# Optimization experiments

Measured on AMD Instinct MI355X. Metric: run time of the kernel, lower is better.

The kernel has to match this reference:

```python
import jax, jax.numpy as jnp
import numpy as np

HID = 128
N_NODES = 50000
N_EDGES = 640000
N_GRAPHS = 64
N_LAYERS = 3
LN_EPS = 1e-5


def _ln(h, g, b):
    mu = jnp.mean(h, axis=-1, keepdims=True)
    v = jnp.mean(jnp.square(h - mu), axis=-1, keepdims=True)
    return (h - mu) * jax.lax.rsqrt(v + LN_EPS) * g + b


def _mlp2(h, W1, b1, g, be, W2, b2):
    # Linear -> ReLU -> LayerNorm -> (Dropout=identity in eval) -> Linear
    h = _ln(jax.nn.relu(h @ W1.T + b1), g, be)
    return h @ W2.T + b2


def _forward(x, edge_index, batch, axis_W1, axis_b1, axis_g, axis_be, axis_W2, axis_b2, org_W1, org_b1, org_g, org_be, org_W2, org_b2, nin_W, nin_b, conv_W1, conv_b1, conv_g, conv_be, conv_W2, conv_b2, eps, ln_g, ln_b, gate_W1, gate_b1, gate_g, gate_be, gate_W2, gate_b2, head_W1, head_b1, head_g, head_be, head_W2, head_b2):
    axis = x[:, 9:12]
    origin = x[:, 12:15]
    others = jnp.concatenate([x[:, :9], x[:, 15:19]], axis=1)  # [N, 13]
    axis_z = _mlp2(axis, axis_W1, axis_b1, axis_g, axis_be, axis_W2, axis_b2)
    org_z = _mlp2(origin, org_W1, org_b1, org_g, org_be, org_W2, org_b2)
    h = jnp.concatenate([others, axis_z, org_z], axis=1) @ nin_W.T + nin_b  # [N, HID]
    src, dst = edge_index[0], edge_index[1]
    n = x.shape[0]
    for l in range(N_LAYERS):
        res = h
        # GIN: sum-aggregate source features into targets (gather + scatter-add)
        agg = jax.ops.segment_sum(h[src], dst, num_segments=n)
        m = (1.0 + eps[l]) * h + agg
        m = _mlp2(m, conv_W1[l], conv_b1[l], conv_g[l], conv_be[l], conv_W2[l], conv_b2[l])
        h = _ln(jax.nn.relu(m), ln_g[l], ln_b[l]) + res
    # AttentionalAggregation: segment softmax over per-graph node gates
    gate = _mlp2(h, gate_W1, gate_b1, gate_g, gate_be, gate_W2, gate_b2)  # [N, 1]
    gmax = jax.ops.segment_max(gate, batch, num_segments=N_GRAPHS)
    e = jnp.exp(gate - gmax[batch])
    denom = jax.ops.segment_sum(e, batch, num_segments=N_GRAPHS)
    attn = e / denom[batch]
    g = jax.ops.segment_sum(attn * h, batch, num_segments=N_GRAPHS)  # [B, HID]
    logit = _mlp2(g, head_W1, head_b1, head_g, head_be, head_W2, head_b2)[:, 0]
    return logit


def setup_inputs() -> dict:
    key = jax.random.key(0)
    ks = iter(jax.random.split(key, 64))
    nk = lambda: next(ks)
    lin = lambda o, i: jax.random.normal(nk(), (o, i), jnp.float32) / np.float32(np.sqrt(i))
    lin3 = lambda L, o, i: jnp.stack([lin(o, i) for _ in range(L)])
    z = lambda *s: jnp.zeros(s, jnp.float32)
    o = lambda *s: jnp.ones(s, jnp.float32)
    inp = {}
    inp['x'] = jax.random.normal(nk(), (N_NODES, 19), jnp.float32)
    inp['edge_index'] = jax.random.randint(nk(), (2, N_EDGES), 0, N_NODES)
    inp['batch'] = jnp.sort(jax.random.randint(nk(), (N_NODES,), 0, N_GRAPHS))
    for p in ('axis', 'org'):
        inp[p + '_W1'] = lin(16, 3); inp[p + '_b1'] = z(16)
        inp[p + '_g'] = o(16); inp[p + '_be'] = z(16)
        inp[p + '_W2'] = lin(16, 16); inp[p + '_b2'] = z(16)
    inp['nin_W'] = lin(HID, 45); inp['nin_b'] = z(HID)
    inp['conv_W1'] = lin3(N_LAYERS, HID, HID); inp['conv_b1'] = z(N_LAYERS, HID)
    inp['conv_g'] = o(N_LAYERS, HID); inp['conv_be'] = z(N_LAYERS, HID)
    inp['conv_W2'] = lin3(N_LAYERS, HID, HID); inp['conv_b2'] = z(N_LAYERS, HID)
    inp['eps'] = z(N_LAYERS)
    inp['ln_g'] = o(N_LAYERS, HID); inp['ln_b'] = z(N_LAYERS, HID)
    for p in ('gate', 'head'):
        inp[p + '_W1'] = lin(HID // 2, HID); inp[p + '_b1'] = z(HID // 2)
        inp[p + '_g'] = o(HID // 2); inp[p + '_be'] = z(HID // 2)
        inp[p + '_W2'] = lin(1, HID // 2); inp[p + '_b2'] = z(1)
    return inp


def reference(x, edge_index, batch, axis_W1, axis_b1, axis_g, axis_be, axis_W2, axis_b2, org_W1, org_b1, org_g, org_be, org_W2, org_b2, nin_W, nin_b, conv_W1, conv_b1, conv_g, conv_be, conv_W2, conv_b2, eps, ln_g, ln_b, gate_W1, gate_b1, gate_g, gate_be, gate_W2, gate_b2, head_W1, head_b1, head_g, head_be, head_W2, head_b2):
    return _forward(x, edge_index, batch, axis_W1, axis_b1, axis_g, axis_be, axis_W2, axis_b2, org_W1, org_b1, org_g, org_be, org_W2, org_b2, nin_W, nin_b, conv_W1, conv_b1, conv_g, conv_be, conv_W2, conv_b2, eps, ln_g, ln_b, gate_W1, gate_b1, gate_g, gate_be, gate_W2, gate_b2, head_W1, head_b1, head_g, head_be, head_W2, head_b2)
```

## Files before the change

kernel.cpp:

```cpp
#include <hip/hip_runtime.h>

#define N_NODESC 50000
#define N_EDGESC 640000
#define N_GRAPHSC 64
#define HIDC 128
#define LN_EPSF 1e-5f
#define POOL_SPLIT 16
#define NGRID_GB ((N_NODESC + 255) / 256)
#define NGRID64 ((N_NODESC + 63) / 64)
#define PREP_ELEMS (8192 + 49152 + 49152)
#define WPREP_NB ((PREP_ELEMS + 255) / 256)
#define B1C 200
#define BCHUNK 3200
#define NBUK 98
#define WBUK 512

typedef short bf16x8 __attribute__((ext_vector_type(8)));
typedef float f32x4 __attribute__((ext_vector_type(4)));

static __device__ __forceinline__ unsigned ord_enc(float f) {
  unsigned u = __float_as_uint(f);
  return (u & 0x80000000u) ? ~u : (u | 0x80000000u);
}
static __device__ __forceinline__ float ord_dec(unsigned u) {
  return __uint_as_float((u & 0x80000000u) ? (u ^ 0x80000000u) : ~u);
}
static __device__ __forceinline__ unsigned short f2bf(float x) {
  unsigned u = __float_as_uint(x);
  u += 0x7fffu + ((u >> 16) & 1u);
  return (unsigned short)(u >> 16);
}
static __device__ __forceinline__ float bf2f(unsigned short b) {
  return __uint_as_float(((unsigned)b) << 16);
}

static __device__ __forceinline__ void mlp16(float in0, float in1, float in2,
    const float* __restrict__ W1, const float* __restrict__ b1,
    const float* __restrict__ g, const float* __restrict__ be,
    const float* __restrict__ W2, const float* __restrict__ b2,
    float* __restrict__ out) {
  float h[16];
  float s1 = 0.f, s2 = 0.f;
#pragma unroll
  for (int j = 0; j < 16; ++j) {
    float v = b1[j] + W1[j*3+0]*in0 + W1[j*3+1]*in1 + W1[j*3+2]*in2;
    v = fmaxf(v, 0.f);
    h[j] = v; s1 += v; s2 += v*v;
  }
  float mu = s1 * (1.f/16.f);
  float var = fmaxf(s2 * (1.f/16.f) - mu*mu, 0.f);
  float rs = rsqrtf(var + LN_EPSF);
  float z[16];
#pragma unroll
  for (int j = 0; j < 16; ++j) z[j] = (h[j]-mu)*rs*g[j] + be[j];
#pragma unroll
  for (int j = 0; j < 16; ++j) {
    float v = b2[j];
#pragma unroll
    for (int k = 0; k < 16; ++k) v += W2[j*16+k]*z[k];
    out[j] = v;
  }
}

__global__ __launch_bounds__(256) void bin_count_kernel(const int* __restrict__ ei,
    int* __restrict__ counts, const int* __restrict__ batch, int* __restrict__ gstart,
    const float* __restrict__ ninW, unsigned short* __restrict__ ninWb,
    const float* __restrict__ cW1, unsigned short* __restrict__ cW1b,
    const float* __restrict__ cW2, unsigned short* __restrict__ cW2b) {
  const int b = blockIdx.x;
  if (b < B1C) {
    __shared__ int cnt[NBUK];
    for (int i = threadIdx.x; i < NBUK; i += 256) cnt[i] = 0;
    __syncthreads();
    const int e0 = b * BCHUNK;
    const int e1 = e0 + BCHUNK;
    for (int e = e0 + threadIdx.x; e < e1; e += 256)
      atomicAdd(&cnt[ei[N_EDGESC + e] >> 9], 1);
    __syncthreads();
    for (int i = threadIdx.x; i < NBUK; i += 256)
      counts[i * B1C + b] = cnt[i];
  } else if (b < B1C + NGRID_GB) {
    int i = (b - B1C) * 256 + threadIdx.x;
    if (i >= N_NODESC) return;
    int bb_ = batch[i];
    int prev = (i == 0) ? -1 : batch[i-1];
    for (int g = prev + 1; g <= bb_; ++g) gstart[g] = i;
    if (i == N_NODESC - 1) {
      for (int g = bb_ + 1; g <= N_GRAPHSC; ++g) gstart[g] = N_NODESC;
    }
  } else {
    int i = (b - B1C - NGRID_GB) * 256 + threadIdx.x;
    if (i < 8192) {
      int f = i >> 6, k = i & 63;
      ninWb[i] = (k < 45) ? f2bf(ninW[f*45 + k]) : (unsigned short)0;
    } else if (i < 8192 + 49152) {
      int j = i - 8192;
      cW1b[j] = f2bf(cW1[j]);
    } else if (i < PREP_ELEMS) {
      int j = i - 8192 - 49152;
      cW2b[j] = f2bf(cW2[j]);
    }
  }
}

__global__ __launch_bounds__(256) void bin_scanA_kernel(const int* __restrict__ counts,
                                                        int* __restrict__ offl,
                                                        int* __restrict__ btot) {
  const int buk = blockIdx.x, t = threadIdx.x;
  const int lane = t & 63, w = t >> 6;
  int v = (t < B1C) ? counts[buk * B1C + t] : 0;
  const int orig = v;
#pragma unroll
  for (int off = 1; off < 64; off <<= 1) {
    int n = __shfl_up(v, off);
    if (lane >= off) v += n;
  }
  __shared__ int wsum[4];
  if (lane == 63) wsum[w] = v;
  __syncthreads();
  if (t == 0) {
    int run = 0;
#pragma unroll
    for (int k = 0; k < 4; ++k) { int x = wsum[k]; wsum[k] = run; run += x; }
  }
  __syncthreads();
  int incl = v + wsum[w];
  if (t < B1C) offl[buk * B1C + t] = incl - orig;
  if (t == 255) btot[buk] = incl;
}

__global__ __launch_bounds__(128) void bin_scanB_kernel(const int* __restrict__ btot,
                                                        int* __restrict__ bb) {
  const int t = threadIdx.x, lane = t & 63, w = t >> 6;
  int v = (t < NBUK) ? btot[t] : 0;
  const int orig = v;
#pragma unroll
  for (int off = 1; off < 64; off <<= 1) {
    int n = __shfl_up(v, off);
    if (lane >= off) v += n;
  }
  __shared__ int ws2[2];
  if (lane == 63) ws2[w] = v;
  __syncthreads();
  int add = (w == 1) ? ws2[0] : 0;
  int excl = v + add - orig;
  if (t < NBUK) bb[t] = excl;
  if (t == 0) bb[NBUK] = N_EDGESC;
}

__global__ __launch_bounds__(256, 4) void bin_write_enc_kernel(
    const int* __restrict__ ei, const int* __restrict__ offl, const int* __restrict__ bb,
    int2* __restrict__ pairs,
    const float* __restrict__ x,
    const float* __restrict__ aW1, const float* __restrict__ ab1,
    const float* __restrict__ ag,  const float* __restrict__ abe,
    const float* __restrict__ aW2, const float* __restrict__ ab2,
    const float* __restrict__ oW1, const float* __restrict__ ob1,
    const float* __restrict__ og,  const float* __restrict__ obe,
    const float* __restrict__ oW2, const float* __restrict__ ob2,
    const unsigned short* __restrict__ ninWb, const float* __restrict__ ninb,
    unsigned short* __restrict__ Hb) {
  __shared__ unsigned short Ab[64*136];
  const int t = threadIdx.x;

  if (blockIdx.x < B1C) {
    int* cur = (int*)Ab;
    const int blk = blockIdx.x;
    for (int i = t; i < NBUK; i += 256) cur[i] = bb[i] + offl[i * B1C + blk];
    __syncthreads();
    const int e0 = blk * BCHUNK;
    const int e1 = e0 + BCHUNK;
    for (int e = e0 + t; e < e1; e += 256) {
      int s = ei[e], d = ei[N_EDGESC + e];
      int pos = atomicAdd(&cur[d >> 9], 1);
      pairs[pos] = make_int2(s, d);
    }
    return;
  }

  const int nb = (blockIdx.x - B1C) * 64;

  if (t < 192) {
    const int n = t & 63;
    const int gn = nb + n;
    const int grp = t >> 6;
    if (gn < N_NODESC) {
      const float* xr = x + gn * 19;
      if (grp == 0) {
        float z[16];
        mlp16(xr[9], xr[10], xr[11], aW1, ab1, ag, abe, aW2, ab2, z);
#pragma unroll
        for (int k = 0; k < 16; ++k) Ab[n*136 + 13 + k] = f2bf(z[k]);
      } else if (grp == 1) {
        float z[16];
        mlp16(xr[12], xr[13], xr[14], oW1, ob1, og, obe, oW2, ob2, z);
#pragma unroll
        for (int k = 0; k < 16; ++k) Ab[n*136 + 29 + k] = f2bf(z[k]);
      } else {
#pragma unroll
        for (int k = 0; k < 9; ++k) Ab[n*136 + k] = f2bf(xr[k]);
#pragma unroll
        for (int k = 0; k < 4; ++k) Ab[n*136 + 9 + k] = f2bf(xr[15 + k]);
#pragma unroll
        for (int k = 45; k < 64; ++k) Ab[n*136 + k] = 0;
      }
    } else {
      if (grp == 0) {
#pragma unroll
        for (int k = 0; k < 16; ++k) Ab[n*136 + 13 + k] = 0;
      } else if (grp == 1) {
#pragma unroll
        for (int k = 0; k < 16; ++k) Ab[n*136 + 29 + k] = 0;
      } else {
#pragma unroll
        for (int k = 0; k < 13; ++k) Ab[n*136 + k] = 0;
#pragma unroll
        for (int k = 45; k < 64; ++k) Ab[n*136 + k] = 0;
      }
    }
  }
  __syncthreads();

  const int lane = t & 63, wv = t >> 6;
  const int quad = lane >> 4, l16 = lane & 15;
  const int arow = (wv*16 + l16)*136 + quad*8;
  f32x4 acc[8];
#pragma unroll
  for (int ft = 0; ft < 8; ++ft) acc[ft] = (f32x4){0.f,0.f,0.f,0.f};
#pragma unroll
  for (int ks = 0; ks < 2; ++ks) {
    bf16x8 a = *(const bf16x8*)(const void*)&Ab[arow + ks*32];
#pragma unroll
    for (int ft = 0; ft < 8; ++ft) {
      bf16x8 bfr = *(const bf16x8*)&ninWb[(ft*16 + l16)*64 + quad*8 + ks*32];
      acc[ft] = __builtin_amdgcn_mfma_f32_16x16x32_bf16(a, bfr, acc[ft], 0, 0, 0);
    }
  }
  float bbv[8];
#pragma unroll
  for (int ft = 0; ft < 8; ++ft) bbv[ft] = ninb[ft*16 + l16];
  __syncthreads();
#pragma unroll
  for (int r = 0; r < 4; ++r) {
    int nloc = wv*16 + quad*4 + r;
#pragma unroll
    for (int ft = 0; ft < 8; ++ft)
      Ab[nloc*136 + ft*16 + l16] = f2bf(acc[ft][r] + bbv[ft]);
  }
  __syncthreads();
#pragma unroll
  for (int i = 0; i < 4; ++i) {
    int chunk = t + i*256;
    int n = chunk >> 4, c8 = chunk & 15;
    int gn = nb + n;
    if (gn < N_NODESC)
      *(bf16x8*)&Hb[gn*HIDC + c8*8] = *(const bf16x8*)&Ab[n*136 + c8*8];
  }
}

__global__ __launch_bounds__(256) void bucket_build_kernel(const int2* __restrict__ pairs,
    const int* __restrict__ bb, int* __restrict__ rowptr, int* __restrict__ esrc) {
  __shared__ int hist[WBUK];
  __shared__ int wsum[4];
  __shared__ int totS;
  const int b = blockIdx.x, t = threadIdx.x;
  const int lane = t & 63, w = t >> 6;
  const int node0 = b * WBUK;
  for (int i = t; i < WBUK; i += 256) hist[i] = 0;
  __syncthreads();
  const int base = bb[b], end = bb[b + 1];
  for (int p = base + t; p < end; p += 256)
    atomicAdd(&hist[pairs[p].y - node0], 1);
  __syncthreads();
  const int v0 = hist[t], v1 = hist[256 + t];
  int a = v0;
#pragma unroll
  for (int off = 1; off < 64; off <<= 1) {
    int n = __shfl_up(a, off);
    if (lane >= off) a += n;
  }
  if (lane == 63) wsum[w] = a;
  __syncthreads();
  if (t == 0) {
    int run = 0;
#pragma unroll
    for (int k = 0; k < 4; ++k) { int x = wsum[k]; wsum[k] = run; run += x; }
    totS = run;
  }
  __syncthreads();
  const int e0 = a + wsum[w] - v0;
  const int tot0 = totS;
  __syncthreads();
  int c = v1;
#pragma unroll
  for (int off = 1; off < 64; off <<= 1) {
    int n = __shfl_up(c, off);
    if (lane >= off) c += n;
  }
  if (lane == 63) wsum[w] = c;
  __syncthreads();
  if (t == 0) {
    int run = 0;
#pragma unroll
    for (int k = 0; k < 4; ++k) { int x = wsum[k]; wsum[k] = run; run += x; }
  }
  __syncthreads();
  const int e1 = tot0 + c + wsum[w] - v1;
  hist[t] = e0;
  hist[256 + t] = e1;
  const int n0 = node0 + t, n1 = node0 + 256 + t;
  if (n0 < N_NODESC) rowptr[n0] = base + e0;
  if (n1 < N_NODESC) rowptr[n1] = base + e1;
  __syncthreads();
  for (int p = base + t; p < end; p += 256) {
    int2 pr = pairs[p];
    int slot = base + atomicAdd(&hist[pr.y - node0], 1);
    esrc[slot] = pr.x;
  }
  if (b == NBUK - 1 && t == 0) rowptr[N_NODESC] = N_EDGESC;
}

__global__ __launch_bounds__(128) void agg_kernel(const unsigned short* __restrict__ Hb,
    const int* __restrict__ rowptr, const int* __restrict__ esrc,
    const float* __restrict__ epsp, unsigned short* __restrict__ Mb) {
  const int t = threadIdx.x;
  const int c8 = t & 15;
  const int v  = t >> 4;
  const int node = blockIdx.x * 8 + v;
  if (node >= N_NODESC) return;
  const float e1 = 1.0f + epsp[0];
  bf16x8 h = *(const bf16x8*)&Hb[node*HIDC + c8*8];
  float acc[8];
#pragma unroll
  for (int k = 0; k < 8; ++k) acc[k] = 0.f;
  int s = rowptr[node];
  const int e = rowptr[node+1];
  for (; s + 8 <= e; s += 8) {
    int i0 = esrc[s],   i1 = esrc[s+1], i2 = esrc[s+2], i3 = esrc[s+3];
    int i4 = esrc[s+4], i5 = esrc[s+5], i6 = esrc[s+6], i7 = esrc[s+7];
    bf16x8 x0 = *(const bf16x8*)&Hb[i0*HIDC + c8*8];
    bf16x8 x1 = *(const bf16x8*)&Hb[i1*HIDC + c8*8];
    bf16x8 x2 = *(const bf16x8*)&Hb[i2*HIDC + c8*8];
    bf16x8 x3 = *(const bf16x8*)&Hb[i3*HIDC + c8*8];
    bf16x8 x4 = *(const bf16x8*)&Hb[i4*HIDC + c8*8];
    bf16x8 x5 = *(const bf16x8*)&Hb[i5*HIDC + c8*8];
    bf16x8 x6 = *(const bf16x8*)&Hb[i6*HIDC + c8*8];
    bf16x8 x7 = *(const bf16x8*)&Hb[i7*HIDC + c8*8];
#pragma unroll
    for (int k = 0; k < 8; ++k)
      acc[k] += ((bf2f((unsigned short)x0[k]) + bf2f((unsigned short)x1[k]))
               + (bf2f((unsigned short)x2[k]) + bf2f((unsigned short)x3[k])))
              + ((bf2f((unsigned short)x4[k]) + bf2f((unsigned short)x5[k]))
               + (bf2f((unsigned short)x6[k]) + bf2f((unsigned short)x7[k])));
  }
  for (; s + 4 <= e; s += 4) {
    int i0 = esrc[s], i1 = esrc[s+1], i2 = esrc[s+2], i3 = esrc[s+3];
    bf16x8 x0 = *(const bf16x8*)&Hb[i0*HIDC + c8*8];
    bf16x8 x1 = *(const bf16x8*)&Hb[i1*HIDC + c8*8];
    bf16x8 x2 = *(const bf16x8*)&Hb[i2*HIDC + c8*8];
    bf16x8 x3 = *(const bf16x8*)&Hb[i3*HIDC + c8*8];
#pragma unroll
    for (int k = 0; k < 8; ++k)
      acc[k] += (bf2f((unsigned short)x0[k]) + bf2f((unsigned short)x1[k]))
              + (bf2f((unsigned short)x2[k]) + bf2f((unsigned short)x3[k]));
  }
  for (; s < e; ++s) {
    bf16x8 x0 = *(const bf16x8*)&Hb[esrc[s]*HIDC + c8*8];
#pragma unroll
    for (int k = 0; k < 8; ++k) acc[k] += bf2f((unsigned short)x0[k]);
  }
  bf16x8 m8;
#pragma unroll
  for (int k = 0; k < 8; ++k)
    m8[k] = (short)f2bf(e1*bf2f((unsigned short)h[k]) + acc[k]);
  *(bf16x8*)&Mb[node*HIDC + c8*8] = m8;
}

template<bool GATE>
__global__ __launch_bounds__(256, 3) void gemmpair_kernel(
    const unsigned short* __restrict__ Mb,
    const unsigned short* __restrict__ Hin,
    const unsigned short* __restrict__ W1b, const float* __restrict__ b1,
    const float* __restrict__ g1, const float* __restrict__ be1,
    const unsigned short* __restrict__ W2b, const float* __restrict__ b2,
    const float* __restrict__ lng, const float* __restrict__ lnb,
    unsigned short* __restrict__ Hout,
    const float* __restrict__ gW1, const float* __restrict__ gb1,
    const float* __restrict__ glng, const float* __restrict__ glnb,
    const float* __restrict__ gW2, const float* __restrict__ gb2,
    const int* __restrict__ batch, float* __restrict__ gateb,
    unsigned* __restrict__ gmaxu) {
  __shared__ unsigned short Ab[64*136];
  __shared__ unsigned short Wl[128*136];
  __shared__ unsigned sgm[N_GRAPHSC];
  const int t = threadIdx.x;
  const int nb = blockIdx.x * 64;
  if (GATE && t < N_GRAPHSC) sgm[t] = 0u;

#pragma unroll
  for (int i = 0; i < 4; ++i) {
    int chunk = t + i*256;
    int n = chunk >> 4, c8 = chunk & 15;
    int gn = nb + n;
    bf16x8 v = {0,0,0,0,0,0,0,0};
    if (gn < N_NODESC) v = *(const bf16x8*)&Mb[gn*HIDC + c8*8];
    *(bf16x8*)&Ab[n*136 + c8*8] = v;
  }
#pragma unroll
  for (int i = 0; i < 8; ++i) {
    int q = t + i*256;
    int f = q >> 4, c8 = q & 15;
    *(bf16x8*)&Wl[f*136 + c8*8] = *(const bf16x8*)&W1b[f*HIDC + c8*8];
  }
  __syncthreads();

  const int lane = t & 63, wv = t >> 6;
  const int quad = lane >> 4, l16 = lane & 15;
  const int arow = (wv*16 + l16)*136 + quad*8;

  f32x4 acc[8];
#pragma unroll
  for (int ft = 0; ft < 8; ++ft) acc[ft] = (f32x4){0.f,0.f,0.f,0.f};
#pragma unroll
  for (int ks = 0; ks < 4; ++ks) {
    bf16x8 a = *(const bf16x8*)(const void*)&Ab[arow + ks*32];
#pragma unroll
    for (int ft = 0; ft < 8; ++ft) {
      bf16x8 b = *(const bf16x8*)(const void*)&Wl[(ft*16 + l16)*136 + quad*8 + ks*32];
      acc[ft] = __builtin_amdgcn_mfma_f32_16x16x32_bf16(a, b, acc[ft], 0, 0, 0);
    }
  }

  {
    float bbv[8], gg[8], bee[8];
#pragma unroll
    for (int ft = 0; ft < 8; ++ft) {
      int f = ft*16 + l16;
      bbv[ft] = b1[f]; gg[ft] = g1[f]; bee[ft] = be1[f];
    }
    float s1[4] = {0,0,0,0}, s2[4] = {0,0,0,0};
#pragma unroll
    for (int ft = 0; ft < 8; ++ft)
#pragma unroll
      for (int r = 0; r < 4; ++r) {
        float v = fmaxf(acc[ft][r] + bbv[ft], 0.f);
        acc[ft][r] = v; s1[r] += v; s2[r] += v*v;
      }
#pragma unroll
    for (int m = 1; m < 16; m <<= 1)
#pragma unroll
      for (int r = 0; r < 4; ++r) {
        s1[r] += __shfl_xor(s1[r], m);
        s2[r] += __shfl_xor(s2[r], m);
      }
    float mu[4], rs[4];
#pragma unroll
    for (int r = 0; r < 4; ++r) {
      mu[r] = s1[r] * (1.f/128.f);
      float var = fmaxf(s2[r] * (1.f/128.f) - mu[r]*mu[r], 0.f);
      rs[r] = rsqrtf(var + LN_EPSF);
    }
    __syncthreads();
#pragma unroll
    for (int r = 0; r < 4; ++r) {
      int nloc = wv*16 + quad*4 + r;
#pragma unroll
      for (int ft = 0; ft < 8; ++ft) {
        float o = (acc[ft][r] - mu[r])*rs[r]*gg[ft] + bee[ft];
        Ab[nloc*136 + ft*16 + l16] = f2bf(o);
      }
    }
  }
#pragma unroll
  for (int i = 0; i < 8; ++i) {
    int q = t + i*256;
    int f = q >> 4, c8 = q & 15;
    *(bf16x8*)&Wl[f*136 + c8*8] = *(const bf16x8*)&W2b[f*HIDC + c8*8];
  }
  __syncthreads();

#pragma unroll
  for (int ft = 0; ft < 8; ++ft) acc[ft] = (f32x4){0.f,0.f,0.f,0.f};
#pragma unroll
  for (int ks = 0; ks < 4; ++ks) {
    bf16x8 a = *(const bf16x8*)(const void*)&Ab[arow + ks*32];
#pragma unroll
    for (int ft = 0; ft < 8; ++ft) {
      bf16x8 b = *(const bf16x8*)(const void*)&Wl[(ft*16 + l16)*136 + quad*8 + ks*32];
      acc[ft] = __builtin_amdgcn_mfma_f32_16x16x32_bf16(a, b, acc[ft], 0, 0, 0);
    }
  }

  {
    float bbv[8], gg[8], bee[8];
#pragma unroll
    for (int ft = 0; ft < 8; ++ft) {
      int f = ft*16 + l16;
      bbv[ft] = b2[f]; gg[ft] = lng[f]; bee[ft] = lnb[f];
    }
    float s1[4] = {0,0,0,0}, s2[4] = {0,0,0,0};
#pragma unroll
    for (int ft = 0; ft < 8; ++ft)
#pragma unroll
      for (int r = 0; r < 4; ++r) {
        float v = fmaxf(acc[ft][r] + bbv[ft], 0.f);
        acc[ft][r] = v; s1[r] += v; s2[r] += v*v;
      }
#pragma unroll
    for (int m = 1; m < 16; m <<= 1)
#pragma unroll
      for (int r = 0; r < 4; ++r) {
        s1[r] += __shfl_xor(s1[r], m);
        s2[r] += __shfl_xor(s2[r], m);
      }
    float mu[4], rs[4];
#pragma unroll
    for (int r = 0; r < 4; ++r) {
      mu[r] = s1[r] * (1.f/128.f);
      float var = fmaxf(s2[r] * (1.f/128.f) - mu[r]*mu[r], 0.f);
      rs[r] = rsqrtf(var + LN_EPSF);
    }
    __syncthreads();
#pragma unroll
    for (int r = 0; r < 4; ++r) {
      int nloc = wv*16 + quad*4 + r;
#pragma unroll
      for (int ft = 0; ft < 8; ++ft) {
        float o = (acc[ft][r] - mu[r])*rs[r]*gg[ft] + bee[ft];
        Ab[nloc*136 + ft*16 + l16] = f2bf(o);
      }
    }
  }
  __syncthreads();
#pragma unroll
  for (int i = 0; i < 4; ++i) {
    int chunk = t + i*256;
    int n = chunk >> 4, cc = chunk & 15;
    int gn = nb + n;
    bf16x8 o8 = {0,0,0,0,0,0,0,0};
    if (gn < N_NODESC) {
      bf16x8 vv = *(const bf16x8*)&Ab[n*136 + cc*8];
      bf16x8 rr = *(const bf16x8*)&Hin[gn*HIDC + cc*8];
#pragma unroll
      for (int k = 0; k < 8; ++k)
        o8[k] = (short)f2bf(bf2f((unsigned short)vv[k]) + bf2f((unsigned short)rr[k]));
      *(bf16x8*)&Hout[gn*HIDC + cc*8] = o8;
    }
    if (GATE) *(bf16x8*)&Ab[n*136 + cc*8] = o8;
  }

  if (GATE) {
#pragma unroll
    for (int i = 0; i < 8; ++i) {
      int q = t + i*256;
      int f = q >> 5, c4 = q & 31;
      float4 v = *(const float4*)&gW1[f*HIDC + c4*4];
      ushort4 hh;
      hh.x = f2bf(v.x); hh.y = f2bf(v.y); hh.z = f2bf(v.z); hh.w = f2bf(v.w);
      *(ushort4*)&Wl[f*136 + c4*4] = hh;
    }
    __syncthreads();

    f32x4 gacc[4];
#pragma unroll
    for (int ft = 0; ft < 4; ++ft) gacc[ft] = (f32x4){0.f,0.f,0.f,0.f};
#pragma unroll
    for (int ks = 0; ks < 4; ++ks) {
      bf16x8 a = *(const bf16x8*)(const void*)&Ab[arow + ks*32];
#pragma unroll
      for (int ft = 0; ft < 4; ++ft) {
        bf16x8 b = *(const bf16x8*)(const void*)&Wl[(ft*16 + l16)*136 + quad*8 + ks*32];
        gacc[ft] = __builtin_amdgcn_mfma_f32_16x16x32_bf16(a, b, gacc[ft], 0, 0, 0);
      }
    }

    float bbv[4], gg[4], bee[4], w2v[4];
#pragma unroll
    for (int ft = 0; ft < 4; ++ft) {
      int f = ft*16 + l16;
      bbv[ft] = gb1[f]; gg[ft] = glng[f]; bee[ft] = glnb[f]; w2v[ft] = gW2[f];
    }
    float s1[4] = {0,0,0,0}, s2[4] = {0,0,0,0};
#pragma unroll
    for (int ft = 0; ft < 4; ++ft)
#pragma unroll
      for (int r = 0; r < 4; ++r) {
        float v = fmaxf(gacc[ft][r] + bbv[ft], 0.f);
        gacc[ft][r] = v; s1[r] += v; s2[r] += v*v;
      }
#pragma unroll
    for (int m = 1; m < 16; m <<= 1)
#pragma unroll
      for (int r = 0; r < 4; ++r) {
        s1[r] += __shfl_xor(s1[r], m);
        s2[r] += __shfl_xor(s2[r], m);
      }
    float pd[4];
#pragma unroll
    for (int r = 0; r < 4; ++r) {
      float mu = s1[r] * (1.f/64.f);
      float var = fmaxf(s2[r] * (1.f/64.f) - mu*mu, 0.f);
      float rs = rsqrtf(var + LN_EPSF);
      float p = 0.f;
#pragma unroll
      for (int ft = 0; ft < 4; ++ft)
        p += ((gacc[ft][r] - mu)*rs*gg[ft] + bee[ft]) * w2v[ft];
      pd[r] = p;
    }
#pragma unroll
    for (int m = 1; m < 16; m <<= 1)
#pragma unroll
      for (int r = 0; r < 4; ++r) pd[r] += __shfl_xor(pd[r], m);
    if (l16 == 0) {
      float b2v = gb2[0];
#pragma unroll
      for (int r = 0; r < 4; ++r) {
        int node = nb + wv*16 + quad*4 + r;
        if (node < N_NODESC) {
          float gv = pd[r] + b2v;
          gateb[node] = gv;
          atomicMax(&sgm[batch[node]], ord_enc(gv));
        }
      }
    }
    __syncthreads();
    if (t < N_GRAPHSC && sgm[t] != 0u) atomicMax(&gmaxu[t], sgm[t]);
  }
}

__global__ __launch_bounds__(256) void pool_kernel(const unsigned short* __restrict__ Hb,
    const float* __restrict__ gateb, const int* __restrict__ gstart,
    const unsigned* __restrict__ gmaxu, float* __restrict__ S,
    float* __restrict__ denom) {
  const int g    = blockIdx.x / POOL_SPLIT;
  const int part = blockIdx.x % POOL_SPLIT;
  const int s0 = gstart[g], s1 = gstart[g+1];
  const int cnt = s1 - s0;
  const int chunk = (cnt + POOL_SPLIT - 1) / POOL_SPLIT;
  int lo = s0 + part * chunk;
  int hi = lo + chunk; if (hi > s1) hi = s1;
  const int t = threadIdx.x;
  const int c8 = t & 15;
  const int v  = t >> 4;
  const float gm = ord_dec(gmaxu[g]);
  float acc[8];
#pragma unroll
  for (int k = 0; k < 8; ++k) acc[k] = 0.f;
  float de = 0.f;
  for (int n = lo + v; n < hi; n += 16) {
    float e = expf(gateb[n] - gm);
    bf16x8 hv = *(const bf16x8*)&Hb[n*HIDC + c8*8];
#pragma unroll
    for (int k = 0; k < 8; ++k) acc[k] += e * bf2f((unsigned short)hv[k]);
    if (c8 == 0) de += e;
  }
  __shared__ float sacc[16*128];
  __shared__ float sden[16];
#pragma unroll
  for (int k = 0; k < 8; ++k) sacc[v*128 + c8*8 + k] = acc[k];
  if (c8 == 0) sden[v] = de;
  __syncthreads();
  if (t < 128) {
    float s = 0.f;
#pragma unroll
    for (int vv = 0; vv < 16; ++vv) s += sacc[vv*128 + t];
    atomicAdd(&S[g*HIDC + t], s);
  }
  if (t == 0) {
    float d = 0.f;
#pragma unroll
    for (int vv = 0; vv < 16; ++vv) d += sden[vv];
    atomicAdd(&denom[g], d);
  }
}

__global__ __launch_bounds__(64) void head_kernel(const float* __restrict__ S,
    const float* __restrict__ denom, const float* __restrict__ W1,
    const float* __restrict__ b1, const float* __restrict__ g,
    const float* __restrict__ be, const float* __restrict__ W2,
    const float* __restrict__ b2, float* __restrict__ out) {
  const int gr = blockIdx.x;
  const int j = threadIdx.x;
  const float inv = 1.0f / denom[gr];
  float v = b1[j];
  for (int k = 0; k < HIDC; ++k) v += (S[gr*HIDC + k] * inv) * W1[j*HIDC + k];
  v = fmaxf(v, 0.f);
  float s1 = v, s2 = v*v;
  for (int off = 32; off; off >>= 1) { s1 += __shfl_xor(s1, off); s2 += __shfl_xor(s2, off); }
  float mu = s1 * (1.f/64.f);
  float var = fmaxf(s2 * (1.f/64.f) - mu*mu, 0.f);
  float rs = rsqrtf(var + LN_EPSF);
  float z = (v-mu)*rs*g[j] + be[j];
  float p = z * W2[j];
  for (int off = 32; off; off >>= 1) p += __shfl_xor(p, off);
  if (j == 0) out[gr] = p + b2[0];
}

extern "C" void kernel_launch(void* const* d_in, const int* in_sizes, int n_in,
                              void* d_out, int out_size, void* d_ws, size_t ws_size,
                              hipStream_t stream) {
  (void)in_sizes; (void)n_in; (void)out_size; (void)ws_size;
  const float* x     = (const float*)d_in[0];
  const int*   ei    = (const int*)d_in[1];
  const int*   batch = (const int*)d_in[2];
  const float* aW1 = (const float*)d_in[3];
  const float* ab1 = (const float*)d_in[4];
  const float* ag  = (const float*)d_in[5];
  const float* abe = (const float*)d_in[6];
  const float* aW2 = (const float*)d_in[7];
  const float* ab2 = (const float*)d_in[8];
  const float* oW1 = (const float*)d_in[9];
  const float* ob1 = (const float*)d_in[10];
  const float* og  = (const float*)d_in[11];
  const float* obe = (const float*)d_in[12];
  const float* oW2 = (const float*)d_in[13];
  const float* ob2 = (const float*)d_in[14];
  const float* ninW = (const float*)d_in[15];
  const float* ninb = (const float*)d_in[16];
  const float* cW1 = (const float*)d_in[17];
  const float* cb1 = (const float*)d_in[18];
  const float* cg  = (const float*)d_in[19];
  const float* cbe = (const float*)d_in[20];
  const float* cW2 = (const float*)d_in[21];
  const float* cb2 = (const float*)d_in[22];
  const float* eps = (const float*)d_in[23];
  const float* lng = (const float*)d_in[24];
  const float* lnb = (const float*)d_in[25];
  const float* gW1 = (const float*)d_in[26];
  const float* gb1 = (const float*)d_in[27];
  const float* gg  = (const float*)d_in[28];
  const float* gbe = (const float*)d_in[29];
  const float* gW2 = (const float*)d_in[30];
  const float* gb2 = (const float*)d_in[31];
  const float* hW1 = (const float*)d_in[32];
  const float* hb1 = (const float*)d_in[33];
  const float* hg  = (const float*)d_in[34];
  const float* hbe = (const float*)d_in[35];
  const float* hW2 = (const float*)d_in[36];
  const float* hb2 = (const float*)d_in[37];

  char* ws = (char*)d_ws;
  unsigned short* Ha = (unsigned short*)(ws + 0);
  unsigned short* Hc = (unsigned short*)(ws + 12800000);
  unsigned short* Mb = (unsigned short*)(ws + 25600000);
  int2* pairs  = (int2*)(ws + 25600000);
  int* counts  = (int*)(ws + 30720000);
  int* offl    = (int*)(ws + 30800000);
  int* btot    = (int*)(ws + 30880000);
  int* bb      = (int*)(ws + 30881024);
  float* gateb = (float*)(ws + 38400000);
  float* S     = (float*)(ws + 38800000);
  float* denom = (float*)(ws + 38832768);
  unsigned* gmaxu = (unsigned*)(ws + 38833024);
  int* rowptr  = (int*)(ws + 38833280);
  int* esrc    = (int*)(ws + 39233284);
  int* gstart  = (int*)(ws + 41793540);
  unsigned short* ninWb = (unsigned short*)(ws + 41800000);
  unsigned short* cW1b  = (unsigned short*)(ws + 41816384);
  unsigned short* cW2b  = (unsigned short*)(ws + 41914688);

  hipMemsetAsync(S, 0, 33280, stream);

  bin_count_kernel<<<B1C + NGRID_GB + WPREP_NB, 256, 0, stream>>>(
      ei, counts, batch, gstart, ninW, ninWb, cW1, cW1b, cW2, cW2b);
  bin_scanA_kernel<<<NBUK, 256, 0, stream>>>(counts, offl, btot);
  bin_scanB_kernel<<<1, 128, 0, stream>>>(btot, bb);
  bin_write_enc_kernel<<<B1C + NGRID64, 256, 0, stream>>>(
      ei, offl, bb, pairs,
      x, aW1, ab1, ag, abe, aW2, ab2,
      oW1, ob1, og, obe, oW2, ob2,
      ninWb, ninb, Ha);
  bucket_build_kernel<<<NBUK, 256, 0, stream>>>(pairs, bb, rowptr, esrc);

  unsigned short* cur = Ha;
  unsigned short* nxt = Hc;
  for (int l = 0; l < 3; ++l) {
    agg_kernel<<<(N_NODESC + 7) / 8, 128, 0, stream>>>(cur, rowptr, esrc, eps + l, Mb);
    if (l < 2) {
      gemmpair_kernel<false><<<NGRID64, 256, 0, stream>>>(
          Mb, cur,
          cW1b + l*HIDC*HIDC, cb1 + l*HIDC, cg + l*HIDC, cbe + l*HIDC,
          cW2b + l*HIDC*HIDC, cb2 + l*HIDC, lng + l*HIDC, lnb + l*HIDC,
          nxt,
          gW1, gb1, gg, gbe, gW2, gb2, batch, gateb, gmaxu);
    } else {
      gemmpair_kernel<true><<<NGRID64, 256, 0, stream>>>(
          Mb, cur,
          cW1b + l*HIDC*HIDC, cb1 + l*HIDC, cg + l*HIDC, cbe + l*HIDC,
          cW2b + l*HIDC*HIDC, cb2 + l*HIDC, lng + l*HIDC, lnb + l*HIDC,
          nxt,
          gW1, gb1, gg, gbe, gW2, gb2, batch, gateb, gmaxu);
    }
    unsigned short* tmp = cur; cur = nxt; nxt = tmp;
  }

  pool_kernel<<<N_GRAPHSC * POOL_SPLIT, 256, 0, stream>>>(Hc, gateb, gstart, gmaxu, S, denom);
  head_kernel<<<N_GRAPHSC, 64, 0, stream>>>(S, denom, hW1, hb1, hg, hbe, hW2, hb2,
                                            (float*)d_out);
}
```

Before: 331.8 us.

## Fuse neighbor aggregation into per-layer GEMM kernel and read weights from global

Merges the separate aggregation kernel into the MLP GEMM kernel, so each 64-node block gathers its neighbor sums straight into shared memory. This removes the M buffer round trip through global memory and three kernel launches. Weight tiles are no longer staged in shared memory; MFMA B fragments are loaded directly from global (L2-cached), which cuts LDS use and raises the occupancy hint to 4. The trade-offs are fewer threads in flight for the latency-bound gather (782 blocks of 256 versus 6250 blocks of 128) and repeated global weight reads per wave.

```diff
diff --git a/kernel.cpp b/kernel.cpp
--- a/kernel.cpp
+++ b/kernel.cpp
@@ -320,66 +320,11 @@
   if (b == NBUK - 1 && t == 0) rowptr[N_NODESC] = N_EDGESC;
 }
 
-__global__ __launch_bounds__(128) void agg_kernel(const unsigned short* __restrict__ Hb,
+template<bool GATE>
+__global__ __launch_bounds__(256, 4) void layer_kernel(
+    const unsigned short* __restrict__ Hin,
     const int* __restrict__ rowptr, const int* __restrict__ esrc,
-    const float* __restrict__ epsp, unsigned short* __restrict__ Mb) {
-  const int t = threadIdx.x;
-  const int c8 = t & 15;
-  const int v  = t >> 4;
-  const int node = blockIdx.x * 8 + v;
-  if (node >= N_NODESC) return;
-  const float e1 = 1.0f + epsp[0];
-  bf16x8 h = *(const bf16x8*)&Hb[node*HIDC + c8*8];
-  float acc[8];
-#pragma unroll
-  for (int k = 0; k < 8; ++k) acc[k] = 0.f;
-  int s = rowptr[node];
-  const int e = rowptr[node+1];
-  for (; s + 8 <= e; s += 8) {
-    int i0 = esrc[s],   i1 = esrc[s+1], i2 = esrc[s+2], i3 = esrc[s+3];
-    int i4 = esrc[s+4], i5 = esrc[s+5], i6 = esrc[s+6], i7 = esrc[s+7];
-    bf16x8 x0 = *(const bf16x8*)&Hb[i0*HIDC + c8*8];
-    bf16x8 x1 = *(const bf16x8*)&Hb[i1*HIDC + c8*8];
-    bf16x8 x2 = *(const bf16x8*)&Hb[i2*HIDC + c8*8];
-    bf16x8 x3 = *(const bf16x8*)&Hb[i3*HIDC + c8*8];
-    bf16x8 x4 = *(const bf16x8*)&Hb[i4*HIDC + c8*8];
-    bf16x8 x5 = *(const bf16x8*)&Hb[i5*HIDC + c8*8];
-    bf16x8 x6 = *(const bf16x8*)&Hb[i6*HIDC + c8*8];
-    bf16x8 x7 = *(const bf16x8*)&Hb[i7*HIDC + c8*8];
-#pragma unroll
-    for (int k = 0; k < 8; ++k)
-      acc[k] += ((bf2f((unsigned short)x0[k]) + bf2f((unsigned short)x1[k]))
-               + (bf2f((unsigned short)x2[k]) + bf2f((unsigned short)x3[k])))
-              + ((bf2f((unsigned short)x4[k]) + bf2f((unsigned short)x5[k]))
-               + (bf2f((unsigned short)x6[k]) + bf2f((unsigned short)x7[k])));
-  }
-  for (; s + 4 <= e; s += 4) {
-    int i0 = esrc[s], i1 = esrc[s+1], i2 = esrc[s+2], i3 = esrc[s+3];
-    bf16x8 x0 = *(const bf16x8*)&Hb[i0*HIDC + c8*8];
-    bf16x8 x1 = *(const bf16x8*)&Hb[i1*HIDC + c8*8];
-    bf16x8 x2 = *(const bf16x8*)&Hb[i2*HIDC + c8*8];
-    bf16x8 x3 = *(const bf16x8*)&Hb[i3*HIDC + c8*8];
-#pragma unroll
-    for (int k = 0; k < 8; ++k)
-      acc[k] += (bf2f((unsigned short)x0[k]) + bf2f((unsigned short)x1[k]))
-              + (bf2f((unsigned short)x2[k]) + bf2f((unsigned short)x3[k]));
-  }
-  for (; s < e; ++s) {
-    bf16x8 x0 = *(const bf16x8*)&Hb[esrc[s]*HIDC + c8*8];
-#pragma unroll
-    for (int k = 0; k < 8; ++k) acc[k] += bf2f((unsigned short)x0[k]);
-  }
-  bf16x8 m8;
-#pragma unroll
-  for (int k = 0; k < 8; ++k)
-    m8[k] = (short)f2bf(e1*bf2f((unsigned short)h[k]) + acc[k]);
-  *(bf16x8*)&Mb[node*HIDC + c8*8] = m8;
-}
-
-template<bool GATE>
-__global__ __launch_bounds__(256, 3) void gemmpair_kernel(
-    const unsigned short* __restrict__ Mb,
-    const unsigned short* __restrict__ Hin,
+    const float* __restrict__ epsp,
     const unsigned short* __restrict__ W1b, const float* __restrict__ b1,
     const float* __restrict__ g1, const float* __restrict__ be1,
     const unsigned short* __restrict__ W2b, const float* __restrict__ b2,
@@ -391,26 +336,67 @@
     const int* __restrict__ batch, float* __restrict__ gateb,
     unsigned* __restrict__ gmaxu) {
   __shared__ unsigned short Ab[64*136];
-  __shared__ unsigned short Wl[128*136];
   __shared__ unsigned sgm[N_GRAPHSC];
   const int t = threadIdx.x;
   const int nb = blockIdx.x * 64;
   if (GATE && t < N_GRAPHSC) sgm[t] = 0u;
 
-#pragma unroll
-  for (int i = 0; i < 4; ++i) {
-    int chunk = t + i*256;
-    int n = chunk >> 4, c8 = chunk & 15;
-    int gn = nb + n;
-    bf16x8 v = {0,0,0,0,0,0,0,0};
-    if (gn < N_NODESC) v = *(const bf16x8*)&Mb[gn*HIDC + c8*8];
-    *(bf16x8*)&Ab[n*136 + c8*8] = v;
-  }
-#pragma unroll
-  for (int i = 0; i < 8; ++i) {
-    int q = t + i*256;
-    int f = q >> 4, c8 = q & 15;
-    *(bf16x8*)&Wl[f*136 + c8*8] = *(const bf16x8*)&W1b[f*HIDC + c8*8];
+  {
+    const float e1 = 1.0f + epsp[0];
+    const int c8 = t & 15;
+    const int nv = t >> 4;
+#pragma unroll
+    for (int p = 0; p < 4; ++p) {
+      const int n = p*16 + nv;
+      const int gn = nb + n;
+      bf16x8 m8 = {0,0,0,0,0,0,0,0};
+      if (gn < N_NODESC) {
+        bf16x8 h = *(const bf16x8*)&Hin[gn*HIDC + c8*8];
+        float acc[8];
+#pragma unroll
+        for (int k = 0; k < 8; ++k) acc[k] = 0.f;
+        int s = rowptr[gn];
+        const int e = rowptr[gn+1];
+        for (; s + 8 <= e; s += 8) {
+          int i0 = esrc[s],   i1 = esrc[s+1], i2 = esrc[s+2], i3 = esrc[s+3];
+          int i4 = esrc[s+4], i5 = esrc[s+5], i6 = esrc[s+6], i7 = esrc[s+7];
+          bf16x8 x0 = *(const bf16x8*)&Hin[i0*HIDC + c8*8];
+          bf16x8 x1 = *(const bf16x8*)&Hin[i1*HIDC + c8*8];
+          bf16x8 x2 = *(const bf16x8*)&Hin[i2*HIDC + c8*8];
+          bf16x8 x3 = *(const bf16x8*)&Hin[i3*HIDC + c8*8];
+          bf16x8 x4 = *(const bf16x8*)&Hin[i4*HIDC + c8*8];
+          bf16x8 x5 = *(const bf16x8*)&Hin[i5*HIDC + c8*8];
+          bf16x8 x6 = *(const bf16x8*)&Hin[i6*HIDC + c8*8];
+          bf16x8 x7 = *(const bf16x8*)&Hin[i7*HIDC + c8*8];
+#pragma unroll
+          for (int k = 0; k < 8; ++k)
+            acc[k] += ((bf2f((unsigned short)x0[k]) + bf2f((unsigned short)x1[k]))
+                     + (bf2f((unsigned short)x2[k]) + bf2f((unsigned short)x3[k])))
+                    + ((bf2f((unsigned short)x4[k]) + bf2f((unsigned short)x5[k]))
+                     + (bf2f((unsigned short)x6[k]) + bf2f((unsigned short)x7[k])));
+        }
+        for (; s + 4 <= e; s += 4) {
+          int i0 = esrc[s], i1 = esrc[s+1], i2 = esrc[s+2], i3 = esrc[s+3];
+          bf16x8 x0 = *(const bf16x8*)&Hin[i0*HIDC + c8*8];
+          bf16x8 x1 = *(const bf16x8*)&Hin[i1*HIDC + c8*8];
+          bf16x8 x2 = *(const bf16x8*)&Hin[i2*HIDC + c8*8];
+          bf16x8 x3 = *(const bf16x8*)&Hin[i3*HIDC + c8*8];
+#pragma unroll
+          for (int k = 0; k < 8; ++k)
+            acc[k] += (bf2f((unsigned short)x0[k]) + bf2f((unsigned short)x1[k]))
+                    + (bf2f((unsigned short)x2[k]) + bf2f((unsigned short)x3[k]));
+        }
+        for (; s < e; ++s) {
+          bf16x8 x0 = *(const bf16x8*)&Hin[esrc[s]*HIDC + c8*8];
+#pragma unroll
+          for (int k = 0; k < 8; ++k) acc[k] += bf2f((unsigned short)x0[k]);
+        }
+#pragma unroll
+        for (int k = 0; k < 8; ++k)
+          m8[k] = (short)f2bf(e1*bf2f((unsigned short)h[k]) + acc[k]);
+      }
+      *(bf16x8*)&Ab[n*136 + c8*8] = m8;
+    }
   }
   __syncthreads();
 
@@ -424,11 +410,13 @@
 #pragma unroll
   for (int ks = 0; ks < 4; ++ks) {
     bf16x8 a = *(const bf16x8*)(const void*)&Ab[arow + ks*32];
-#pragma unroll
-    for (int ft = 0; ft < 8; ++ft) {
-      bf16x8 b = *(const bf16x8*)(const void*)&Wl[(ft*16 + l16)*136 + quad*8 + ks*32];
-      acc[ft] = __builtin_amdgcn_mfma_f32_16x16x32_bf16(a, b, acc[ft], 0, 0, 0);
-    }
+    bf16x8 wfr[8];
+#pragma unroll
+    for (int ft = 0; ft < 8; ++ft)
+      wfr[ft] = *(const bf16x8*)&W1b[(ft*16 + l16)*HIDC + quad*8 + ks*32];
+#pragma unroll
+    for (int ft = 0; ft < 8; ++ft)
+      acc[ft] = __builtin_amdgcn_mfma_f32_16x16x32_bf16(a, wfr[ft], acc[ft], 0, 0, 0);
   }
 
   {
@@ -471,12 +459,6 @@
       }
     }
   }
-#pragma unroll
-  for (int i = 0; i < 8; ++i) {
-    int q = t + i*256;
-    int f = q >> 4, c8 = q & 15;
-    *(bf16x8*)&Wl[f*136 + c8*8] = *(const bf16x8*)&W2b[f*HIDC + c8*8];
-  }
   __syncthreads();
 
 #pragma unroll
@@ -484,11 +466,13 @@
 #pragma unroll
   for (int ks = 0; ks < 4; ++ks) {
     bf16x8 a = *(const bf16x8*)(const void*)&Ab[arow + ks*32];
-#pragma unroll
-    for (int ft = 0; ft < 8; ++ft) {
-      bf16x8 b = *(const bf16x8*)(const void*)&Wl[(ft*16 + l16)*136 + quad*8 + ks*32];
-      acc[ft] = __builtin_amdgcn_mfma_f32_16x16x32_bf16(a, b, acc[ft], 0, 0, 0);
-    }
+    bf16x8 wfr[8];
+#pragma unroll
+    for (int ft = 0; ft < 8; ++ft)
+      wfr[ft] = *(const bf16x8*)&W2b[(ft*16 + l16)*HIDC + quad*8 + ks*32];
+#pragma unroll
+    for (int ft = 0; ft < 8; ++ft)
+      acc[ft] = __builtin_amdgcn_mfma_f32_16x16x32_bf16(a, wfr[ft], acc[ft], 0, 0, 0);
   }
 
   {
@@ -550,15 +534,6 @@
   }
 
   if (GATE) {
-#pragma unroll
-    for (int i = 0; i < 8; ++i) {
-      int q = t + i*256;
-      int f = q >> 5, c4 = q & 31;
-      float4 v = *(const float4*)&gW1[f*HIDC + c4*4];
-      ushort4 hh;
-      hh.x = f2bf(v.x); hh.y = f2bf(v.y); hh.z = f2bf(v.z); hh.w = f2bf(v.w);
-      *(ushort4*)&Wl[f*136 + c4*4] = hh;
-    }
     __syncthreads();
 
     f32x4 gacc[4];
@@ -569,8 +544,15 @@
       bf16x8 a = *(const bf16x8*)(const void*)&Ab[arow + ks*32];
 #pragma unroll
       for (int ft = 0; ft < 4; ++ft) {
-        bf16x8 b = *(const bf16x8*)(const void*)&Wl[(ft*16 + l16)*136 + quad*8 + ks*32];
-        gacc[ft] = __builtin_amdgcn_mfma_f32_16x16x32_bf16(a, b, gacc[ft], 0, 0, 0);
+        const float* wp = &gW1[(ft*16 + l16)*HIDC + quad*8 + ks*32];
+        float4 w0 = *(const float4*)wp;
+        float4 w1 = *(const float4*)(wp + 4);
+        bf16x8 wb;
+        wb[0] = (short)f2bf(w0.x); wb[1] = (short)f2bf(w0.y);
+        wb[2] = (short)f2bf(w0.z); wb[3] = (short)f2bf(w0.w);
+        wb[4] = (short)f2bf(w1.x); wb[5] = (short)f2bf(w1.y);
+        wb[6] = (short)f2bf(w1.z); wb[7] = (short)f2bf(w1.w);
+        gacc[ft] = __builtin_amdgcn_mfma_f32_16x16x32_bf16(a, wb, gacc[ft], 0, 0, 0);
       }
     }
 
@@ -742,7 +724,6 @@
   char* ws = (char*)d_ws;
   unsigned short* Ha = (unsigned short*)(ws + 0);
   unsigned short* Hc = (unsigned short*)(ws + 12800000);
-  unsigned short* Mb = (unsigned short*)(ws + 25600000);
   int2* pairs  = (int2*)(ws + 25600000);
   int* counts  = (int*)(ws + 30720000);
   int* offl    = (int*)(ws + 30800000);
@@ -772,27 +753,24 @@
       ninWb, ninb, Ha);
   bucket_build_kernel<<<NBUK, 256, 0, stream>>>(pairs, bb, rowptr, esrc);
 
-  unsigned short* cur = Ha;
-  unsigned short* nxt = Hc;
-  for (int l = 0; l < 3; ++l) {
-    agg_kernel<<<(N_NODESC + 7) / 8, 128, 0, stream>>>(cur, rowptr, esrc, eps + l, Mb);
-    if (l < 2) {
-      gemmpair_kernel<false><<<NGRID64, 256, 0, stream>>>(
-          Mb, cur,
-          cW1b + l*HIDC*HIDC, cb1 + l*HIDC, cg + l*HIDC, cbe + l*HIDC,
-          cW2b + l*HIDC*HIDC, cb2 + l*HIDC, lng + l*HIDC, lnb + l*HIDC,
-          nxt,
-          gW1, gb1, gg, gbe, gW2, gb2, batch, gateb, gmaxu);
-    } else {
-      gemmpair_kernel<true><<<NGRID64, 256, 0, stream>>>(
-          Mb, cur,
-          cW1b + l*HIDC*HIDC, cb1 + l*HIDC, cg + l*HIDC, cbe + l*HIDC,
-          cW2b + l*HIDC*HIDC, cb2 + l*HIDC, lng + l*HIDC, lnb + l*HIDC,
-          nxt,
-          gW1, gb1, gg, gbe, gW2, gb2, batch, gateb, gmaxu);
-    }
-    unsigned short* tmp = cur; cur = nxt; nxt = tmp;
-  }
+  layer_kernel<false><<<NGRID64, 256, 0, stream>>>(
+      Ha, rowptr, esrc, eps + 0,
+      cW1b + 0*HIDC*HIDC, cb1 + 0*HIDC, cg + 0*HIDC, cbe + 0*HIDC,
+      cW2b + 0*HIDC*HIDC, cb2 + 0*HIDC, lng + 0*HIDC, lnb + 0*HIDC,
+      Hc,
+      gW1, gb1, gg, gbe, gW2, gb2, batch, gateb, gmaxu);
+  layer_kernel<false><<<NGRID64, 256, 0, stream>>>(
+      Hc, rowptr, esrc, eps + 1,
+      cW1b + 1*HIDC*HIDC, cb1 + 1*HIDC, cg + 1*HIDC, cbe + 1*HIDC,
+      cW2b + 1*HIDC*HIDC, cb2 + 1*HIDC, lng + 1*HIDC, lnb + 1*HIDC,
+      Ha,
+      gW1, gb1, gg, gbe, gW2, gb2, batch, gateb, gmaxu);
+  layer_kernel<true><<<NGRID64, 256, 0, stream>>>(
+      Ha, rowptr, esrc, eps + 2,
+      cW1b + 2*HIDC*HIDC, cb1 + 2*HIDC, cg + 2*HIDC, cbe + 2*HIDC,
+      cW2b + 2*HIDC*HIDC, cb2 + 2*HIDC, lng + 2*HIDC, lnb + 2*HIDC,
+      Hc,
+      gW1, gb1, gg, gbe, gW2, gb2, batch, gateb, gmaxu);
 
   pool_kernel<<<N_GRAPHSC * POOL_SPLIT, 256, 0, stream>>>(Hc, gateb, gstart, gmaxu, S, denom);
   head_kernel<<<N_GRAPHSC, 64, 0, stream>>>(S, denom, hW1, hb1, hg, hbe, hW2, hb2,
```

Result: slower. 378.4 us (+14.1%).

## Fuse attention pooling into final GEMM kernel, dropping segment max

Applied to the files above, without the earlier changes.

Fuses the attentional pooling into the last gemmpair kernel. Each block exponentiates its gate values without subtracting the per-graph max and accumulates gated features per graph run into global S and denom with atomics. This removes the pool kernel, the gstart computation, the gate buffer and the separate memset, which was folded into bin_count. In exchange the softmax loses max-subtraction, so large gate values can overflow, and many more global atomics go to a small hot array. It also relies on Ab holding the final H at that point.

```diff
diff --git a/kernel.cpp b/kernel.cpp
--- a/kernel.cpp
+++ b/kernel.cpp
@@ -5,8 +5,6 @@
 #define N_GRAPHSC 64
 #define HIDC 128
 #define LN_EPSF 1e-5f
-#define POOL_SPLIT 16
-#define NGRID_GB ((N_NODESC + 255) / 256)
 #define NGRID64 ((N_NODESC + 63) / 64)
 #define PREP_ELEMS (8192 + 49152 + 49152)
 #define WPREP_NB ((PREP_ELEMS + 255) / 256)
@@ -18,13 +16,6 @@
 typedef short bf16x8 __attribute__((ext_vector_type(8)));
 typedef float f32x4 __attribute__((ext_vector_type(4)));
 
-static __device__ __forceinline__ unsigned ord_enc(float f) {
-  unsigned u = __float_as_uint(f);
-  return (u & 0x80000000u) ? ~u : (u | 0x80000000u);
-}
-static __device__ __forceinline__ float ord_dec(unsigned u) {
-  return __uint_as_float((u & 0x80000000u) ? (u ^ 0x80000000u) : ~u);
-}
 static __device__ __forceinline__ unsigned short f2bf(float x) {
   unsigned u = __float_as_uint(x);
   u += 0x7fffu + ((u >> 16) & 1u);
@@ -63,7 +54,8 @@
 }
 
 __global__ __launch_bounds__(256) void bin_count_kernel(const int* __restrict__ ei,
-    int* __restrict__ counts, const int* __restrict__ batch, int* __restrict__ gstart,
+    int* __restrict__ counts,
+    float* __restrict__ Szero,
     const float* __restrict__ ninW, unsigned short* __restrict__ ninWb,
     const float* __restrict__ cW1, unsigned short* __restrict__ cW1b,
     const float* __restrict__ cW2, unsigned short* __restrict__ cW2b) {
@@ -79,17 +71,11 @@
     __syncthreads();
     for (int i = threadIdx.x; i < NBUK; i += 256)
       counts[i * B1C + b] = cnt[i];
-  } else if (b < B1C + NGRID_GB) {
-    int i = (b - B1C) * 256 + threadIdx.x;
-    if (i >= N_NODESC) return;
-    int bb_ = batch[i];
-    int prev = (i == 0) ? -1 : batch[i-1];
-    for (int g = prev + 1; g <= bb_; ++g) gstart[g] = i;
-    if (i == N_NODESC - 1) {
-      for (int g = bb_ + 1; g <= N_GRAPHSC; ++g) gstart[g] = N_NODESC;
-    }
+  } else if (b == B1C) {
+    for (int i = threadIdx.x; i < N_GRAPHSC * HIDC + N_GRAPHSC; i += 256)
+      Szero[i] = 0.f;
   } else {
-    int i = (b - B1C - NGRID_GB) * 256 + threadIdx.x;
+    int i = (b - B1C - 1) * 256 + threadIdx.x;
     if (i < 8192) {
       int f = i >> 6, k = i & 63;
       ninWb[i] = (k < 45) ? f2bf(ninW[f*45 + k]) : (unsigned short)0;
@@ -388,14 +374,14 @@
     const float* __restrict__ gW1, const float* __restrict__ gb1,
     const float* __restrict__ glng, const float* __restrict__ glnb,
     const float* __restrict__ gW2, const float* __restrict__ gb2,
-    const int* __restrict__ batch, float* __restrict__ gateb,
-    unsigned* __restrict__ gmaxu) {
+    const int* __restrict__ batch, float* __restrict__ S,
+    float* __restrict__ denom) {
   __shared__ unsigned short Ab[64*136];
   __shared__ unsigned short Wl[128*136];
-  __shared__ unsigned sgm[N_GRAPHSC];
+  __shared__ float Egate[64];
+  __shared__ int   Sbatch[64];
   const int t = threadIdx.x;
   const int nb = blockIdx.x * 64;
-  if (GATE && t < N_GRAPHSC) sgm[t] = 0u;
 
 #pragma unroll
   for (int i = 0; i < 4; ++i) {
@@ -615,62 +601,46 @@
       float b2v = gb2[0];
 #pragma unroll
       for (int r = 0; r < 4; ++r) {
-        int node = nb + wv*16 + quad*4 + r;
+        int nloc = wv*16 + quad*4 + r;
+        int node = nb + nloc;
         if (node < N_NODESC) {
-          float gv = pd[r] + b2v;
-          gateb[node] = gv;
-          atomicMax(&sgm[batch[node]], ord_enc(gv));
+          Egate[nloc]  = expf(pd[r] + b2v);
+          Sbatch[nloc] = batch[node];
+        } else {
+          Egate[nloc]  = 0.f;
+          Sbatch[nloc] = -1;
         }
       }
     }
     __syncthreads();
-    if (t < N_GRAPHSC && sgm[t] != 0u) atomicMax(&gmaxu[t], sgm[t]);
-  }
-}
-
-__global__ __launch_bounds__(256) void pool_kernel(const unsigned short* __restrict__ Hb,
-    const float* __restrict__ gateb, const int* __restrict__ gstart,
-    const unsigned* __restrict__ gmaxu, float* __restrict__ S,
-    float* __restrict__ denom) {
-  const int g    = blockIdx.x / POOL_SPLIT;
-  const int part = blockIdx.x % POOL_SPLIT;
-  const int s0 = gstart[g], s1 = gstart[g+1];
-  const int cnt = s1 - s0;
-  const int chunk = (cnt + POOL_SPLIT - 1) / POOL_SPLIT;
-  int lo = s0 + part * chunk;
-  int hi = lo + chunk; if (hi > s1) hi = s1;
-  const int t = threadIdx.x;
-  const int c8 = t & 15;
-  const int v  = t >> 4;
-  const float gm = ord_dec(gmaxu[g]);
-  float acc[8];
-#pragma unroll
-  for (int k = 0; k < 8; ++k) acc[k] = 0.f;
-  float de = 0.f;
-  for (int n = lo + v; n < hi; n += 16) {
-    float e = expf(gateb[n] - gm);
-    bf16x8 hv = *(const bf16x8*)&Hb[n*HIDC + c8*8];
-#pragma unroll
-    for (int k = 0; k < 8; ++k) acc[k] += e * bf2f((unsigned short)hv[k]);
-    if (c8 == 0) de += e;
-  }
-  __shared__ float sacc[16*128];
-  __shared__ float sden[16];
-#pragma unroll
-  for (int k = 0; k < 8; ++k) sacc[v*128 + c8*8 + k] = acc[k];
-  if (c8 == 0) sden[v] = de;
-  __syncthreads();
-  if (t < 128) {
-    float s = 0.f;
-#pragma unroll
-    for (int vv = 0; vv < 16; ++vv) s += sacc[vv*128 + t];
-    atomicAdd(&S[g*HIDC + t], s);
-  }
-  if (t == 0) {
-    float d = 0.f;
-#pragma unroll
-    for (int vv = 0; vv < 16; ++vv) d += sden[vv];
-    atomicAdd(&denom[g], d);
+
+    if (t < HIDC) {
+      const int f = t;
+      float accS = 0.f;
+      int curG = Sbatch[0];
+#pragma unroll 4
+      for (int n = 0; n < 64; ++n) {
+        int g = Sbatch[n];
+        if (g != curG) {
+          if (curG >= 0) atomicAdd(&S[curG*HIDC + f], accS);
+          accS = 0.f; curG = g;
+        }
+        if (g >= 0) accS += Egate[n] * bf2f((unsigned short)Ab[n*136 + f]);
+      }
+      if (curG >= 0) atomicAdd(&S[curG*HIDC + f], accS);
+    } else if (t == HIDC) {
+      float accD = 0.f;
+      int curG = Sbatch[0];
+      for (int n = 0; n < 64; ++n) {
+        int g = Sbatch[n];
+        if (g != curG) {
+          if (curG >= 0) atomicAdd(&denom[curG], accD);
+          accD = 0.f; curG = g;
+        }
+        if (g >= 0) accD += Egate[n];
+      }
+      if (curG >= 0) atomicAdd(&denom[curG], accD);
+    }
   }
 }
 
@@ -748,21 +718,16 @@
   int* offl    = (int*)(ws + 30800000);
   int* btot    = (int*)(ws + 30880000);
   int* bb      = (int*)(ws + 30881024);
-  float* gateb = (float*)(ws + 38400000);
   float* S     = (float*)(ws + 38800000);
   float* denom = (float*)(ws + 38832768);
-  unsigned* gmaxu = (unsigned*)(ws + 38833024);
   int* rowptr  = (int*)(ws + 38833280);
   int* esrc    = (int*)(ws + 39233284);
-  int* gstart  = (int*)(ws + 41793540);
   unsigned short* ninWb = (unsigned short*)(ws + 41800000);
   unsigned short* cW1b  = (unsigned short*)(ws + 41816384);
   unsigned short* cW2b  = (unsigned short*)(ws + 41914688);
 
-  hipMemsetAsync(S, 0, 33280, stream);
-
-  bin_count_kernel<<<B1C + NGRID_GB + WPREP_NB, 256, 0, stream>>>(
-      ei, counts, batch, gstart, ninW, ninWb, cW1, cW1b, cW2, cW2b);
+  bin_count_kernel<<<B1C + 1 + WPREP_NB, 256, 0, stream>>>(
+      ei, counts, S, ninW, ninWb, cW1, cW1b, cW2, cW2b);
   bin_scanA_kernel<<<NBUK, 256, 0, stream>>>(counts, offl, btot);
   bin_scanB_kernel<<<1, 128, 0, stream>>>(btot, bb);
   bin_write_enc_kernel<<<B1C + NGRID64, 256, 0, stream>>>(
@@ -782,19 +747,18 @@
           cW1b + l*HIDC*HIDC, cb1 + l*HIDC, cg + l*HIDC, cbe + l*HIDC,
           cW2b + l*HIDC*HIDC, cb2 + l*HIDC, lng + l*HIDC, lnb + l*HIDC,
           nxt,
-          gW1, gb1, gg, gbe, gW2, gb2, batch, gateb, gmaxu);
+          gW1, gb1, gg, gbe, gW2, gb2, batch, S, denom);
     } else {
       gemmpair_kernel<true><<<NGRID64, 256, 0, stream>>>(
           Mb, cur,
           cW1b + l*HIDC*HIDC, cb1 + l*HIDC, cg + l*HIDC, cbe + l*HIDC,
           cW2b + l*HIDC*HIDC, cb2 + l*HIDC, lng + l*HIDC, lnb + l*HIDC,
           nxt,
-          gW1, gb1, gg, gbe, gW2, gb2, batch, gateb, gmaxu);
+          gW1, gb1, gg, gbe, gW2, gb2, batch, S, denom);
     }
     unsigned short* tmp = cur; cur = nxt; nxt = tmp;
   }
 
-  pool_kernel<<<N_GRAPHSC * POOL_SPLIT, 256, 0, stream>>>(Hc, gateb, gstart, gmaxu, S, denom);
   head_kernel<<<N_GRAPHSC, 64, 0, stream>>>(S, denom, hW1, hb1, hg, hbe, hW2, hb2,
                                             (float*)d_out);
 }
```

Result: no change. 327.7 us (-1.2%).
